# Kernel tuning notes

Measured on AMD Instinct MI355X. Metric: run time of the kernel, lower is better.

Reference implementation:

```python
import jax, jax.numpy as jnp
import numpy as np

EPS_PDIST = 1e-8  # torch PairwiseDistance adds eps to (x1 - x2)


def setup_inputs() -> dict:
    key = jax.random.key(0)
    B, T, D = 8, 4096, 256
    student_output = jax.random.normal(key, (B, T, D), dtype=jnp.float32)
    return {"student_output": student_output}


def reference(student_output) -> jnp.ndarray:
    x = student_output.astype(jnp.float32)  # autocast disabled -> fp32
    B, T, D = x.shape
    eps = 1e-8  # forward default arg
    # pairwise inner products [B, T, T]
    dots = jnp.einsum('btd,bsd->bts', x, x)
    # fill diagonal with -1 so a point is never its own NN
    diag = jnp.eye(T, dtype=bool)
    dots = jnp.where(diag[None, :, :], jnp.float32(-1.0), dots)
    I = jnp.argmax(dots, axis=2)  # [B, T] int
    # gather nearest neighbors: neighbors[b, t] = x[b, I[b, t]]
    neighbors = jnp.take_along_axis(x, I[:, :, None], axis=1)  # [B, T, D]
    # PairwiseDistance(2, eps=1e-8): ||x - y + eps||_2
    diff = x - neighbors + EPS_PDIST
    distances = jnp.sqrt(jnp.sum(diff * diff, axis=-1))  # [B, T]
    loss = -jnp.mean(jnp.log(distances + eps))
    return loss
```

## Files before the change

### kernel.cpp

```cpp
#include <hip/hip_runtime.h>
#include <math.h>


#define Bq 8
#define Tq 4096
#define Dq 256
#define TW 32
#define NT 32
#define S_QUART 1024
#define WTILEB (TW * 256)
#define BIAS 256.0f

typedef __attribute__((ext_vector_type(4))) float f32x4;
typedef unsigned int u32;

__device__ __forceinline__ void gload_lds16(const void* g, void* l) {
    typedef __attribute__((address_space(1))) const unsigned int gu32;
    typedef __attribute__((address_space(3))) unsigned int lu32;
    __builtin_amdgcn_global_load_lds((gu32*)g, (lu32*)l, 16, 0, 0);
}

__global__ void cvt_kernel(const float* __restrict__ x, uint2* __restrict__ xq,
                           u32* __restrict__ keys, float* __restrict__ out) {
    const int i = blockIdx.x * blockDim.x + threadIdx.x;
    const float4* in = (const float4*)x;
    float4 v0 = in[2 * i], v1 = in[2 * i + 1];
    u32 a = 0, b = 0, c = 0, d = 0;
    asm volatile("v_cvt_pk_fp8_f32 %0, %1, %2" : "+v"(a) : "v"(v0.x), "v"(v0.y));
    asm volatile("v_cvt_pk_fp8_f32 %0, %1, %2" : "+v"(b) : "v"(v0.z), "v"(v0.w));
    asm volatile("v_cvt_pk_fp8_f32 %0, %1, %2" : "+v"(c) : "v"(v1.x), "v"(v1.y));
    asm volatile("v_cvt_pk_fp8_f32 %0, %1, %2" : "+v"(d) : "v"(v1.z), "v"(v1.w));
    uint2 o;
    o.x = (a & 0xffffu) | (b << 16);
    o.y = (c & 0xffffu) | (d << 16);
    xq[i] = o;
    if (i < Bq * Tq) keys[i] = 0;
    if (i == 0) *out = 0.f;
}

__global__ __launch_bounds__(512, 2)
void argmax_kernel(const unsigned char* __restrict__ xq, u32* __restrict__ keys) {
    const int bid   = blockIdx.x;
    const int batch = bid & 7;
    const int rt    = (bid >> 3) & 7;
    const int sq    = bid >> 6;
    const int tid   = threadIdx.x;
    const int lane  = tid & 63;
    const int wave  = tid >> 6;
    const int lrow  = lane & 15;
    const int lk    = lane >> 4;

    const unsigned char* xB = xq + (size_t)batch * Tq * Dq;
    const int rowBase = rt * 512 + wave * 64;
    const int sBase = sq * S_QUART;

    __shared__ char smem[8 * 2 * WTILEB];
    char* myl = smem + wave * (2 * WTILEB);

    long afrag[8][4];
#pragma unroll
    for (int mi = 0; mi < 4; ++mi) {
        const unsigned char* rp = xB + (size_t)(rowBase + mi * 16 + lrow) * Dq + lk * 8;
#pragma unroll
        for (int kk = 0; kk < 8; ++kk)
            afrag[kk][mi] = *(const long*)(rp + kk * 32);
    }

    int g_off[8];
#pragma unroll
    for (int it = 0; it < 8; ++it) {
        const int ls = it * 1024 + lane * 16;
        const int s_local = ls >> 8;
        const int q = ls & 255;
        g_off[it] = s_local * 256 + (q ^ ((s_local & 15) << 4));
    }
    int dsoff[8];
#pragma unroll
    for (int kk = 0; kk < 8; ++kk)
        dsoff[kk] = lrow * 256 + ((kk * 32 + lk * 8) ^ ((lrow & 15) << 4));

    auto STAGE = [&](int t, int buf) {
        const unsigned char* gsrc = xB + (size_t)(sBase + t * TW) * 256;
        char* lb = myl + buf * WTILEB;
#pragma unroll
        for (int it = 0; it < 8; ++it)
            gload_lds16(gsrc + g_off[it], lb + it * 1024 + lane * 16);
    };

    u32 bkey[4][4];
#pragma unroll
    for (int mi = 0; mi < 4; ++mi)
#pragma unroll
        for (int j = 0; j < 4; ++j) bkey[mi][j] = 0u;

    STAGE(0, 0);
    asm volatile("s_waitcnt vmcnt(0)" ::: "memory");
    __builtin_amdgcn_sched_barrier(0);

    for (int t = 0; t < NT; ++t) {
        if (t + 1 < NT) {
            STAGE(t + 1, (t + 1) & 1);
            asm volatile("s_waitcnt vmcnt(8)" ::: "memory");
        } else {
            asm volatile("s_waitcnt vmcnt(0)" ::: "memory");
        }
        __builtin_amdgcn_sched_barrier(0);

        const char* lb = myl + (t & 1) * WTILEB;

#pragma unroll
        for (int p = 0; p < 2; ++p) {
            f32x4 acc[4];
#pragma unroll
            for (int mi = 0; mi < 4; ++mi)
                acc[mi] = (f32x4){BIAS, BIAS, BIAS, BIAS};

#pragma unroll
            for (int kk = 0; kk < 8; ++kk) {
                const long bfr = *(const long*)(lb + dsoff[kk] + p * 4096);
#pragma unroll
                for (int mi = 0; mi < 4; ++mi)
                    acc[mi] = __builtin_amdgcn_mfma_f32_16x16x32_fp8_fp8(
                        afrag[kk][mi], bfr, acc[mi], 0, 0, 0);
            }

            const int colB = sBase + t * TW + p * 16;
            const int sv = colB + lrow;
            const u32 invs = (u32)(~sv) & 0xFFFu;
            if (colB < rowBase + 64 && rowBase < colB + 16) {
#pragma unroll
                for (int mi = 0; mi < 4; ++mi) {
                    const int tbase = rowBase + mi * 16 + lk * 4;
#pragma unroll
                    for (int j = 0; j < 4; ++j) {
                        u32 key = (__float_as_uint(acc[mi][j]) & ~0xFFFu) | invs;
                        key = (sv == tbase + j) ? 0u : key;
                        bkey[mi][j] = max(bkey[mi][j], key);
                    }
                }
            } else {
#pragma unroll
                for (int mi = 0; mi < 4; ++mi) {
#pragma unroll
                    for (int j = 0; j < 4; ++j) {
                        const u32 key = (__float_as_uint(acc[mi][j]) & ~0xFFFu) | invs;
                        bkey[mi][j] = max(bkey[mi][j], key);
                    }
                }
            }
        }
    }

#pragma unroll
    for (int mi = 0; mi < 4; ++mi) {
#pragma unroll
        for (int j = 0; j < 4; ++j) {
            u32 k = bkey[mi][j];
#pragma unroll
            for (int m = 8; m >= 1; m >>= 1)
                k = max(k, (u32)__shfl_xor((int)k, m, 64));
            if (lrow == 0) {
                const int row = rowBase + mi * 16 + lk * 4 + j;
                atomicMax(keys + batch * Tq + row, k);
            }
        }
    }
}

__global__ void loss_kernel(const float* __restrict__ x, const u32* __restrict__ keys,
                            float* __restrict__ out) {
    const int lane = threadIdx.x & 63;
    const int wave = threadIdx.x >> 6;
    const int gw = blockIdx.x * 4 + wave;
    float lsum = 0.f;

    for (int row = gw; row < Bq * Tq; row += 2048) {
        const int b = row >> 12;
        const int t = row & (Tq - 1);
        const int s = (int)((~keys[row]) & 0xFFFu);
        const float4* xt = (const float4*)(x + ((size_t)b * Tq + t) * Dq);
        const float4* xs = (const float4*)(x + ((size_t)b * Tq + s) * Dq);
        float4 a = xt[lane];
        float4 c = xs[lane];
        float dx = a.x - c.x + 1e-8f;
        float dy = a.y - c.y + 1e-8f;
        float dz = a.z - c.z + 1e-8f;
        float dw = a.w - c.w + 1e-8f;
        float sum = dx * dx + dy * dy + dz * dz + dw * dw;
#pragma unroll
        for (int m = 32; m >= 1; m >>= 1)
            sum += __shfl_xor(sum, m, 64);
        if (lane == 0)
            lsum += logf(sqrtf(sum) + 1e-8f);
    }

    __shared__ float red[4];
    if (lane == 0) red[wave] = lsum;
    __syncthreads();
    if (threadIdx.x == 0) {
        float s = red[0] + red[1] + red[2] + red[3];
        atomicAdd(out, -s * (1.0f / (Bq * Tq)));
    }
}

extern "C" void kernel_launch(void* const* d_in, const int* in_sizes, int n_in,
                              void* d_out, int out_size, void* d_ws, size_t ws_size,
                              hipStream_t stream) {
    const float* x = (const float*)d_in[0];
    float* out = (float*)d_out;

    unsigned char* xq = (unsigned char*)d_ws;
    u32* keys = (u32*)((char*)d_ws + (size_t)Bq * Tq * Dq);

    const int n8 = Bq * Tq * Dq / 8;
    cvt_kernel<<<n8 / 256, 256, 0, stream>>>(x, (uint2*)xq, keys, out);
    argmax_kernel<<<256, 512, 0, stream>>>(xq, keys);
    loss_kernel<<<512, 256, 0, stream>>>(x, keys, out);
}
```

Baseline: 84.67 us.

## Switch argmax GEMM to 32x32x64 scaled fp8 MFMA on gfx950

Replaces the 16x16x32 fp8 MFMA tiles with the gfx950 mfma_scale 32x32x64 f8f6f4 instruction, using unit scales. This restructures the A-fragment registers, the LDS read offsets (two 16-byte reads per 32-byte B fragment), the accumulator-to-row mapping and the cross-lane reduction for the 32-wide layout. The aim is fewer, larger matrix instructions with higher per-instruction throughput and fewer LDS reads. The trade-offs are more accumulator registers and a 32-lane shuffle reduction in the epilogue.

```diff
diff --git a/kernel.cpp b/kernel.cpp
--- a/kernel.cpp
+++ b/kernel.cpp
@@ -10,14 +10,21 @@
 #define S_QUART 1024
 #define WTILEB (TW * 256)
 #define BIAS 256.0f
-
-typedef __attribute__((ext_vector_type(4))) float f32x4;
+#define SCL 0x7F7F7F7F
+
+typedef __attribute__((ext_vector_type(4))) int i32x4;
+typedef __attribute__((ext_vector_type(8))) int i32x8;
+typedef __attribute__((ext_vector_type(16))) float f32x16;
 typedef unsigned int u32;
 
 __device__ __forceinline__ void gload_lds16(const void* g, void* l) {
     typedef __attribute__((address_space(1))) const unsigned int gu32;
     typedef __attribute__((address_space(3))) unsigned int lu32;
     __builtin_amdgcn_global_load_lds((gu32*)g, (lu32*)l, 16, 0, 0);
+}
+
+__device__ __forceinline__ i32x8 pack32B(i32x4 lo, i32x4 hi) {
+    return __builtin_shufflevector(lo, hi, 0, 1, 2, 3, 4, 5, 6, 7);
 }
 
 __global__ void cvt_kernel(const float* __restrict__ x, uint2* __restrict__ xq,
@@ -47,8 +54,8 @@
     const int tid   = threadIdx.x;
     const int lane  = tid & 63;
     const int wave  = tid >> 6;
-    const int lrow  = lane & 15;
-    const int lk    = lane >> 4;
+    const int l31   = lane & 31;
+    const int lh    = lane >> 5;
 
     const unsigned char* xB = xq + (size_t)batch * Tq * Dq;
     const int rowBase = rt * 512 + wave * 64;
@@ -57,13 +64,14 @@
     __shared__ char smem[8 * 2 * WTILEB];
     char* myl = smem + wave * (2 * WTILEB);
 
-    long afrag[8][4];
-#pragma unroll
-    for (int mi = 0; mi < 4; ++mi) {
-        const unsigned char* rp = xB + (size_t)(rowBase + mi * 16 + lrow) * Dq + lk * 8;
-#pragma unroll
-        for (int kk = 0; kk < 8; ++kk)
-            afrag[kk][mi] = *(const long*)(rp + kk * 32);
+    i32x8 afrag[4][2];
+#pragma unroll
+    for (int rb = 0; rb < 2; ++rb) {
+        const unsigned char* rp = xB + (size_t)(rowBase + rb * 32 + l31) * Dq + lh * 32;
+#pragma unroll
+        for (int kc = 0; kc < 4; ++kc)
+            afrag[kc][rb] = pack32B(*(const i32x4*)(rp + kc * 64),
+                                    *(const i32x4*)(rp + kc * 64 + 16));
     }
 
     int g_off[8];
@@ -74,10 +82,16 @@
         const int q = ls & 255;
         g_off[it] = s_local * 256 + (q ^ ((s_local & 15) << 4));
     }
-    int dsoff[8];
-#pragma unroll
-    for (int kk = 0; kk < 8; ++kk)
-        dsoff[kk] = lrow * 256 + ((kk * 32 + lk * 8) ^ ((lrow & 15) << 4));
+    int dsoff0[4], dsoff1[4];
+    {
+        const int mask = (l31 & 15) << 4;
+#pragma unroll
+        for (int kc = 0; kc < 4; ++kc) {
+            const int q = kc * 64 + lh * 32;
+            dsoff0[kc] = l31 * 256 + (q ^ mask);
+            dsoff1[kc] = l31 * 256 + ((q + 16) ^ mask);
+        }
+    }
 
     auto STAGE = [&](int t, int buf) {
         const unsigned char* gsrc = xB + (size_t)(sBase + t * TW) * 256;
@@ -87,11 +101,11 @@
             gload_lds16(gsrc + g_off[it], lb + it * 1024 + lane * 16);
     };
 
-    u32 bkey[4][4];
-#pragma unroll
-    for (int mi = 0; mi < 4; ++mi)
-#pragma unroll
-        for (int j = 0; j < 4; ++j) bkey[mi][j] = 0u;
+    u32 bkey[2][16];
+#pragma unroll
+    for (int rb = 0; rb < 2; ++rb)
+#pragma unroll
+        for (int r = 0; r < 16; ++r) bkey[rb][r] = 0u;
 
     STAGE(0, 0);
     asm volatile("s_waitcnt vmcnt(0)" ::: "memory");
@@ -108,59 +122,58 @@
 
         const char* lb = myl + (t & 1) * WTILEB;
 
-#pragma unroll
-        for (int p = 0; p < 2; ++p) {
-            f32x4 acc[4];
-#pragma unroll
-            for (int mi = 0; mi < 4; ++mi)
-                acc[mi] = (f32x4){BIAS, BIAS, BIAS, BIAS};
-
-#pragma unroll
-            for (int kk = 0; kk < 8; ++kk) {
-                const long bfr = *(const long*)(lb + dsoff[kk] + p * 4096);
-#pragma unroll
-                for (int mi = 0; mi < 4; ++mi)
-                    acc[mi] = __builtin_amdgcn_mfma_f32_16x16x32_fp8_fp8(
-                        afrag[kk][mi], bfr, acc[mi], 0, 0, 0);
-            }
-
-            const int colB = sBase + t * TW + p * 16;
-            const int sv = colB + lrow;
-            const u32 invs = (u32)(~sv) & 0xFFFu;
-            if (colB < rowBase + 64 && rowBase < colB + 16) {
-#pragma unroll
-                for (int mi = 0; mi < 4; ++mi) {
-                    const int tbase = rowBase + mi * 16 + lk * 4;
-#pragma unroll
-                    for (int j = 0; j < 4; ++j) {
-                        u32 key = (__float_as_uint(acc[mi][j]) & ~0xFFFu) | invs;
-                        key = (sv == tbase + j) ? 0u : key;
-                        bkey[mi][j] = max(bkey[mi][j], key);
-                    }
-                }
-            } else {
-#pragma unroll
-                for (int mi = 0; mi < 4; ++mi) {
-#pragma unroll
-                    for (int j = 0; j < 4; ++j) {
-                        const u32 key = (__float_as_uint(acc[mi][j]) & ~0xFFFu) | invs;
-                        bkey[mi][j] = max(bkey[mi][j], key);
-                    }
+        f32x16 acc[2];
+#pragma unroll
+        for (int rb = 0; rb < 2; ++rb)
+#pragma unroll
+            for (int r = 0; r < 16; ++r) acc[rb][r] = BIAS;
+
+#pragma unroll
+        for (int kc = 0; kc < 4; ++kc) {
+            const i32x8 bfr = pack32B(*(const i32x4*)(lb + dsoff0[kc]),
+                                      *(const i32x4*)(lb + dsoff1[kc]));
+            acc[0] = __builtin_amdgcn_mfma_scale_f32_32x32x64_f8f6f4(
+                afrag[kc][0], bfr, acc[0], 0, 0, 0, SCL, 0, SCL);
+            acc[1] = __builtin_amdgcn_mfma_scale_f32_32x32x64_f8f6f4(
+                afrag[kc][1], bfr, acc[1], 0, 0, 0, SCL, 0, SCL);
+        }
+
+        const int colB = sBase + t * TW;
+        const int sv = colB + l31;
+        const u32 invs = (u32)(~sv) & 0xFFFu;
+        if (colB < rowBase + 64 && rowBase < colB + 32) {
+#pragma unroll
+            for (int rb = 0; rb < 2; ++rb) {
+#pragma unroll
+                for (int r = 0; r < 16; ++r) {
+                    const int tj = rowBase + rb * 32 + (r & 3) + 8 * (r >> 2) + 4 * lh;
+                    u32 key = (__float_as_uint(acc[rb][r]) & ~0xFFFu) | invs;
+                    key = (sv == tj) ? 0u : key;
+                    bkey[rb][r] = max(bkey[rb][r], key);
                 }
             }
-        }
-    }
-
-#pragma unroll
-    for (int mi = 0; mi < 4; ++mi) {
-#pragma unroll
-        for (int j = 0; j < 4; ++j) {
-            u32 k = bkey[mi][j];
-#pragma unroll
-            for (int m = 8; m >= 1; m >>= 1)
+        } else {
+#pragma unroll
+            for (int rb = 0; rb < 2; ++rb) {
+#pragma unroll
+                for (int r = 0; r < 16; ++r) {
+                    const u32 key = (__float_as_uint(acc[rb][r]) & ~0xFFFu) | invs;
+                    bkey[rb][r] = max(bkey[rb][r], key);
+                }
+            }
+        }
+    }
+
+#pragma unroll
+    for (int rb = 0; rb < 2; ++rb) {
+#pragma unroll
+        for (int r = 0; r < 16; ++r) {
+            u32 k = bkey[rb][r];
+#pragma unroll
+            for (int m = 16; m >= 1; m >>= 1)
                 k = max(k, (u32)__shfl_xor((int)k, m, 64));
-            if (lrow == 0) {
-                const int row = rowBase + mi * 16 + lk * 4 + j;
+            if (l31 == 0) {
+                const int row = rowBase + rb * 32 + (r & 3) + 8 * (r >> 2) + 4 * lh;
                 atomicMax(keys + batch * Tq + row, k);
             }
         }
```

Measured after the change: 71.22 us. 15.9% less time.
